# Optimization experiments

Measured on AMD Instinct MI355X. Metric: run time of the kernel, lower is better.

Reference implementation:

```python
import jax, jax.numpy as jnp
import numpy as np

MUL = 128
LS = [0, 1, 2]
D1 = [MUL * (2 * l + 1) for l in LS]            # per-irrep dims of x1 / out: 128, 384, 640
D2 = [2 * l + 1 for l in LS]                    # per-irrep dims of x2 (mul=1): 1, 3, 5
O1 = np.concatenate([[0], np.cumsum(D1)])       # offsets into x1 / out
O2 = np.concatenate([[0], np.cumsum(D2)])       # offsets into x2
PATHS = [(l1, l2, lo) for l1 in LS for l2 in LS for lo in LS
         if abs(l1 - l2) <= lo <= l1 + l2]      # 15 sorted 'uvw' instructions
DIM_OUT = int(sum(D1))

def _count():
    # fan-in count per output position: each 'uvw' path adds mul_1*mul_2 = 128
    c = np.zeros(DIM_OUT, dtype=np.float32)
    for (_, _, lo) in PATHS:
        c[O1[lo]:O1[lo] + D1[lo]] += MUL * 1
    return np.maximum(c, 1.0)

COUNT = jnp.asarray(_count())

def setup_inputs() -> dict:
    key = jax.random.key(0)
    ks = jax.random.split(key, 3 + len(PATHS))
    N = 16384
    inp = {
        "x1": jax.random.normal(ks[0], (N, int(sum(D1))), jnp.float32),
        "x2": jax.random.normal(ks[1], (N, int(sum(D2))), jnp.float32),
        "ws": jax.random.normal(ks[2], (len(PATHS), MUL, 1, MUL), jnp.float32),
    }
    for p, (l1, l2, lo) in enumerate(PATHS):
        inp[f"c{p}"] = jax.random.normal(ks[3 + p], (2 * l1 + 1, 2 * l2 + 1, 2 * lo + 1), jnp.float32)
    return inp

def _forward(x1, x2, ws, cs):
    N = x1.shape[0]
    out = jnp.zeros((N, DIM_OUT), x1.dtype)
    for p, (l1, l2, lo) in enumerate(PATHS):
        # s1: [N, mul1, 2l1+1]; s2: [N, mul2=1, 2l2+1]
        s1 = x1[:, int(O1[l1]):int(O1[l1] + D1[l1])].reshape(N, MUL, 2 * l1 + 1)
        s2 = x2[:, int(O2[l2]):int(O2[l2] + D2[l2])].reshape(N, 1, 2 * l2 + 1)
        # weighted CG contraction: ws[p] [u,v,w], cs[p] [i,j,k]
        contrib = jnp.einsum('uvw,ijk,zui,zvj->zwk', ws[p], cs[p], s1, s2)
        out = out.at[:, int(O1[lo]):int(O1[lo] + D1[lo])].add(contrib.reshape(N, D1[lo]))
    # fan-in (component) normalization
    return out / jnp.sqrt(COUNT)

def reference(x1, x2, ws, c0, c1, c2, c3, c4, c5, c6, c7, c8, c9, c10, c11, c12, c13, c14):
    cs = [c0, c1, c2, c3, c4, c5, c6, c7, c8, c9, c10, c11, c12, c13, c14]
    return _forward(x1, x2, ws, cs)
```

## Files before the change

### kernel.cpp

```cpp
#include <hip/hip_runtime.h>
#include <hip/hip_bf16.h>

typedef float f32x4 __attribute__((ext_vector_type(4)));
typedef short bf16x8 __attribute__((ext_vector_type(8)));

#define ZT 16
#define TL_COLS 160
#define TL_RING (TL_COLS * 128)
#define YL_BUF 640

constexpr int cL1[15]  = {0,0,0,1,1,1,1,1,1,2,2,2,2,2,2};
constexpr int cL2[15]  = {0,1,2,0,1,1,1,2,2,0,1,1,2,2,2};
constexpr int cLO[15]  = {0,1,2,1,0,1,2,1,2,2,1,2,0,1,2};
constexpr int cCSZ[15] = {1,9,25,9,9,27,45,45,75,25,45,75,25,75,125};
constexpr int cCOFF[15]= {0,1,10,35,44,53,80,125,170,245,270,315,390,415,490};
constexpr int cO1[3] = {0,128,512};
constexpr int cO2[3] = {0,1,4};

constexpr int cSEQ[15] = {0,4,12, 1,3,5,7,10,13, 2,6,8,9,11,14};

struct CP { const float* p[15]; };

__device__ __forceinline__ ushort f2bf(float f) {
    union { __hip_bfloat16 h; ushort u; } c;
    c.h = __float2bfloat16(f);
    return c.u;
}

__global__ void prep_w(const float* __restrict__ ws, ushort* __restrict__ wb) {
    __shared__ float lds[64 * 132];
    const int p = blockIdx.x;
    const int tid = threadIdx.x;
    const float* src = ws + (size_t)p * 16384;
    ushort* dst = wb + (size_t)p * 16384;
    for (int half = 0; half < 2; ++half) {
        for (int i = tid; i < 8192; i += 256) {
            int u = i >> 7, w = i & 127;
            lds[u * 132 + w] = src[(half * 64 + u) * 128 + w];
        }
        __syncthreads();
        for (int i = tid; i < 8192; i += 256) {
            int w = i >> 6, u = i & 63;
            dst[w * 128 + half * 64 + u] = f2bf(lds[u * 132 + w]);
        }
        __syncthreads();
    }
}

template<int P>
__device__ __forceinline__ void compute_y(int tid, const float* __restrict__ cl,
                                          const float* __restrict__ x2l,
                                          float* __restrict__ ybuf) {
    constexpr int l2 = cL2[P], lo = cLO[P];
    constexpr int d1 = 2*cL1[P]+1, d2 = 2*l2+1, dO = 2*lo+1;
    constexpr int ipad = (d1 == 5) ? 8 : 4;
    constexpr int span_pad = dO * ipad;
    constexpr int ny = ZT * span_pad;
    for (int idx = tid; idx < ny; idx += 256) {
        const int z = idx / span_pad, rem = idx - z * span_pad;
        const int k = rem / ipad, i = rem & (ipad - 1);
        float s = 0.f;
        if (i < d1) {
            #pragma unroll
            for (int j = 0; j < d2; ++j)
                s += cl[cCOFF[P] + (i*d2 + j)*dO + k] * x2l[z*9 + cO2[l2] + j];
        }
        ybuf[idx] = s;
    }
}

template<int L1>
__device__ __forceinline__ void load_x1(const float* __restrict__ x1, int z0,
                                        int wv, int lane, float (&x1c)[4][2][5]) {
    #pragma unroll
    for (int r = 0; r < 4; ++r) {
        const float* b = x1 + (size_t)(z0 + wv*4 + r) * 1152;
        if constexpr (L1 == 0) {
            const float2 t = *reinterpret_cast<const float2*>(b + 2*lane);
            x1c[r][0][0] = t.x; x1c[r][1][0] = t.y;
        } else if constexpr (L1 == 1) {
            float f6[6];
            #pragma unroll
            for (int j = 0; j < 3; ++j) {
                const float2 t = *reinterpret_cast<const float2*>(b + 128 + 6*lane + 2*j);
                f6[2*j] = t.x; f6[2*j + 1] = t.y;
            }
            #pragma unroll
            for (int i = 0; i < 3; ++i) { x1c[r][0][i] = f6[i]; x1c[r][1][i] = f6[3+i]; }
        } else {
            float f10[10];
            #pragma unroll
            for (int j = 0; j < 5; ++j) {
                const float2 t = *reinterpret_cast<const float2*>(b + 512 + 10*lane + 2*j);
                f10[2*j] = t.x; f10[2*j + 1] = t.y;
            }
            #pragma unroll
            for (int i = 0; i < 5; ++i) { x1c[r][0][i] = f10[i]; x1c[r][1][i] = f10[5+i]; }
        }
    }
}

template<int S>
__device__ __forceinline__ void path_iter(
    int tid, const float* __restrict__ x1, int z0,
    const ushort* __restrict__ Wb, const float* __restrict__ Wsrc, int use_prep,
    float (&x1c)[4][2][5],
    float* __restrict__ yl, ushort* __restrict__ Tl,
    const float* __restrict__ cl, const float* __restrict__ x2l,
    f32x4 (&acc)[5][2])
{
    constexpr int P = cSEQ[S];
    constexpr int l1 = cL1[P], lo = cLO[P];
    constexpr int d1 = 2*l1+1, dO = 2*lo+1;
    constexpr int ipad = (d1 == 5) ? 8 : 4;
    constexpr int span_pad = dO * ipad;
    constexpr int roff = (S & 1) ? 80 : 0;
    const int lane = tid & 63, wv = tid >> 6;
    const int g = lane >> 4, m = lane & 15;

    ushort* Tcur = Tl + roff * 128;
    const float* ycur = yl + (S & 1) * YL_BUF;

    if constexpr (S == 0 || cL1[cSEQ[S - 1]] != l1)
        load_x1<l1>(x1, z0, wv, lane, x1c);

    {
        const int u0 = 2 * lane;
        #pragma unroll
        for (int r = 0; r < 4; ++r) {
            const int z = wv * 4 + r;
            #pragma unroll
            for (int k = 0; k < dO; ++k) {
                const f32x4 y0 = *reinterpret_cast<const f32x4*>(
                    ycur + z * span_pad + k * ipad);
                float s0 = 0.f, s1 = 0.f;
                #pragma unroll
                for (int i = 0; i < ((d1 < 4) ? d1 : 4); ++i) {
                    s0 += x1c[r][0][i] * y0[i];
                    s1 += x1c[r][1][i] * y0[i];
                }
                if constexpr (d1 == 5) {
                    const float y4 = ycur[z * span_pad + k * ipad + 4];
                    s0 += x1c[r][0][4] * y4;
                    s1 += x1c[r][1][4] * y4;
                }
                const int col = z * dO + k;
                union { uint u32; ushort h[2]; } pk;
                pk.h[0] = f2bf(s0);
                pk.h[1] = f2bf(s1);
                const uint idx = (uint)(col * 128 + u0) ^ (uint)((col & 7) << 3);
                *reinterpret_cast<uint*>(Tcur + idx) = pk.u32;
            }
        }
    }

    bf16x8 aP[2][4];
    if (use_prep) {
        const ushort* wp = Wb + P * 16384;
        #pragma unroll
        for (int nt = 0; nt < 2; ++nt)
        #pragma unroll
        for (int ks = 0; ks < 4; ++ks)
            aP[nt][ks] = *reinterpret_cast<const bf16x8*>(
                wp + (wv*32 + nt*16 + m)*128 + ks*32 + g*8);
    } else {
        const float* wp = Wsrc + P * 16384;
        #pragma unroll
        for (int nt = 0; nt < 2; ++nt)
        #pragma unroll
        for (int ks = 0; ks < 4; ++ks) {
            bf16x8 v;
            #pragma unroll
            for (int e = 0; e < 8; ++e)
                v[e] = (short)f2bf(wp[(ks*32 + g*8 + e)*128 + wv*32 + nt*16 + m]);
            aP[nt][ks] = v;
        }
    }

    if constexpr (S < 14)
        compute_y<cSEQ[S + 1]>(tid, cl, x2l, yl + ((S + 1) & 1) * YL_BUF);

    __syncthreads();

    #pragma unroll
    for (int t = 0; t < dO; ++t) {
        #pragma unroll
        for (int ks = 0; ks < 4; ++ks) {
            const uint idx = (uint)((t*16 + m) * 128 + ks*32 + g*8)
                           ^ (uint)(((t*16 + m) & 7) << 3);
            const bf16x8 a = *reinterpret_cast<const bf16x8*>(Tcur + idx);
            acc[t][0] = __builtin_amdgcn_mfma_f32_16x16x32_bf16(a, aP[0][ks], acc[t][0], 0,0,0);
            acc[t][1] = __builtin_amdgcn_mfma_f32_16x16x32_bf16(a, aP[1][ks], acc[t][1], 0,0,0);
        }
    }
}

template<int LO, bool LAST>
__device__ __forceinline__ void store_pass(const f32x4 (&acc)[5][2], float* __restrict__ out,
                                           float* __restrict__ stage, int z0, int tid)
{
    constexpr int dO = 2*LO + 1;
    constexpr float scale = (LO == 0) ? 0.05103103630798288f
                                      : 0.03608439182435161f;
    const int lane = tid & 63, wv = tid >> 6;
    const int g = lane >> 4, m = lane & 15;
    __syncthreads();
    #pragma unroll
    for (int t = 0; t < dO; ++t)
    #pragma unroll
    for (int r = 0; r < 4; ++r) {
        const int zcol = t*16 + g*4 + r;
        const int z = zcol / dO, k = zcol - z*dO;
        #pragma unroll
        for (int nt = 0; nt < 2; ++nt) {
            const int w = wv*32 + nt*16 + m;
            stage[z*(128*dO) + w*dO + k] = acc[t][nt][r] * scale;
        }
    }
    __syncthreads();
    const float4* src = (const float4*)stage;
    #pragma unroll
    for (int it = 0; it < 2*dO; ++it) {
        const int idx = it * 256 + tid;
        const int z = idx / (32*dO), rem = idx - z*(32*dO);
        ((float4*)(out + (size_t)(z0 + z)*1152 + cO1[LO]))[rem] = src[idx];
    }
    if constexpr (!LAST) __syncthreads();
}

__device__ __forceinline__ void zero_acc(f32x4 (&acc)[5][2]) {
    #pragma unroll
    for (int t = 0; t < 5; ++t)
        #pragma unroll
        for (int nt = 0; nt < 2; ++nt)
            acc[t][nt] = (f32x4){0.f, 0.f, 0.f, 0.f};
}

__global__ __launch_bounds__(256, 2)
void tp_main(const float* __restrict__ x1, const float* __restrict__ x2,
             const float* __restrict__ wsrc, const ushort* __restrict__ wb,
             int use_prep, CP cp, float* __restrict__ out)
{
    __shared__ __align__(16) ushort Tl[TL_RING];
    __shared__ __align__(16) float yl[2 * YL_BUF];
    __shared__ float cl[615];
    __shared__ float x2l[ZT * 9];

    const int tid = threadIdx.x;
    const int z0 = blockIdx.x * ZT;

    #pragma unroll
    for (int p = 0; p < 15; ++p)
        for (int i = tid; i < cCSZ[p]; i += 256) cl[cCOFF[p] + i] = cp.p[p][i];
    for (int i = tid; i < ZT * 9; i += 256) x2l[i] = x2[(size_t)z0 * 9 + i];

    float x1c[4][2][5];
    f32x4 acc[5][2];
    zero_acc(acc);

    __syncthreads();
    compute_y<cSEQ[0]>(tid, cl, x2l, yl);
    __syncthreads();

    float* stage = (float*)Tl;

    path_iter< 0>(tid, x1, z0, wb, wsrc, use_prep, x1c, yl, Tl, cl, x2l, acc);
    path_iter< 1>(tid, x1, z0, wb, wsrc, use_prep, x1c, yl, Tl, cl, x2l, acc);
    path_iter< 2>(tid, x1, z0, wb, wsrc, use_prep, x1c, yl, Tl, cl, x2l, acc);
    store_pass<0, false>(acc, out, stage, z0, tid);
    zero_acc(acc);

    path_iter< 3>(tid, x1, z0, wb, wsrc, use_prep, x1c, yl, Tl, cl, x2l, acc);
    path_iter< 4>(tid, x1, z0, wb, wsrc, use_prep, x1c, yl, Tl, cl, x2l, acc);
    path_iter< 5>(tid, x1, z0, wb, wsrc, use_prep, x1c, yl, Tl, cl, x2l, acc);
    path_iter< 6>(tid, x1, z0, wb, wsrc, use_prep, x1c, yl, Tl, cl, x2l, acc);
    path_iter< 7>(tid, x1, z0, wb, wsrc, use_prep, x1c, yl, Tl, cl, x2l, acc);
    path_iter< 8>(tid, x1, z0, wb, wsrc, use_prep, x1c, yl, Tl, cl, x2l, acc);
    store_pass<1, false>(acc, out, stage, z0, tid);
    zero_acc(acc);

    path_iter< 9>(tid, x1, z0, wb, wsrc, use_prep, x1c, yl, Tl, cl, x2l, acc);
    path_iter<10>(tid, x1, z0, wb, wsrc, use_prep, x1c, yl, Tl, cl, x2l, acc);
    path_iter<11>(tid, x1, z0, wb, wsrc, use_prep, x1c, yl, Tl, cl, x2l, acc);
    path_iter<12>(tid, x1, z0, wb, wsrc, use_prep, x1c, yl, Tl, cl, x2l, acc);
    path_iter<13>(tid, x1, z0, wb, wsrc, use_prep, x1c, yl, Tl, cl, x2l, acc);
    path_iter<14>(tid, x1, z0, wb, wsrc, use_prep, x1c, yl, Tl, cl, x2l, acc);
    store_pass<2, true>(acc, out, stage, z0, tid);
}

extern "C" void kernel_launch(void* const* d_in, const int* in_sizes, int n_in,
                              void* d_out, int out_size, void* d_ws, size_t ws_size,
                              hipStream_t stream) {
    const float* x1 = (const float*)d_in[0];
    const float* x2 = (const float*)d_in[1];
    const float* ws = (const float*)d_in[2];
    CP cp;
    for (int p = 0; p < 15; ++p) cp.p[p] = (const float*)d_in[3 + p];
    float* out = (float*)d_out;

    const int N = in_sizes[0] / 1152;
    const int use_prep = (ws_size >= (size_t)(15 * 128 * 128 * 2)) ? 1 : 0;

    if (use_prep)
        prep_w<<<15, 256, 0, stream>>>(ws, (ushort*)d_ws);
    tp_main<<<N / ZT, 256, 0, stream>>>(x1, x2, ws, (const ushort*)d_ws,
                                        use_prep, cp, out);
}
```

Measured before the change: 104.9 us.

## Stream weight fragments per k-slice and raise occupancy to three blocks per SU

Replaces the eight preloaded weight fragments per stage with a two-register double buffer that fetches the next k-slice while the current one feeds the MFMAs, and reorders the loop to go over k-slices first. The x1 load for the next stage's l1 now happens before the barrier instead of at the start of the next stage. Launch bounds ask for three blocks per CU instead of two. The aim is to cut VGPR pressure so occupancy can rise and global latency can be hidden. In exchange, weight loads now sit on the MFMA critical path, and the tighter register cap may cause spills.

After: 121.4 us. 1.16x slower.

```diff
diff --git a/kernel.cpp b/kernel.cpp
--- a/kernel.cpp
+++ b/kernel.cpp
@@ -121,7 +121,7 @@
     ushort* Tcur = Tl + roff * 128;
     const float* ycur = yl + (S & 1) * YL_BUF;
 
-    if constexpr (S == 0 || cL1[cSEQ[S - 1]] != l1)
+    if constexpr (S == 0)
         load_x1<l1>(x1, z0, wv, lane, x1c);
 
     {
@@ -154,44 +154,61 @@
         }
     }
 
-    bf16x8 aP[2][4];
+    bf16x8 aQ0, aQ1;
     if (use_prep) {
         const ushort* wp = Wb + P * 16384;
-        #pragma unroll
-        for (int nt = 0; nt < 2; ++nt)
-        #pragma unroll
-        for (int ks = 0; ks < 4; ++ks)
-            aP[nt][ks] = *reinterpret_cast<const bf16x8*>(
-                wp + (wv*32 + nt*16 + m)*128 + ks*32 + g*8);
+        aQ0 = *reinterpret_cast<const bf16x8*>(wp + (wv*32 + m)*128 + g*8);
+        aQ1 = *reinterpret_cast<const bf16x8*>(wp + (wv*32 + 16 + m)*128 + g*8);
     } else {
         const float* wp = Wsrc + P * 16384;
-        #pragma unroll
-        for (int nt = 0; nt < 2; ++nt)
-        #pragma unroll
-        for (int ks = 0; ks < 4; ++ks) {
-            bf16x8 v;
-            #pragma unroll
-            for (int e = 0; e < 8; ++e)
-                v[e] = (short)f2bf(wp[(ks*32 + g*8 + e)*128 + wv*32 + nt*16 + m]);
-            aP[nt][ks] = v;
-        }
+        bf16x8 v0, v1;
+        #pragma unroll
+        for (int e = 0; e < 8; ++e) {
+            v0[e] = (short)f2bf(wp[(g*8 + e)*128 + wv*32 + m]);
+            v1[e] = (short)f2bf(wp[(g*8 + e)*128 + wv*32 + 16 + m]);
+        }
+        aQ0 = v0; aQ1 = v1;
     }
 
     if constexpr (S < 14)
         compute_y<cSEQ[S + 1]>(tid, cl, x2l, yl + ((S + 1) & 1) * YL_BUF);
 
-    __syncthreads();
-
-    #pragma unroll
-    for (int t = 0; t < dO; ++t) {
-        #pragma unroll
-        for (int ks = 0; ks < 4; ++ks) {
+    if constexpr (S < 14) {
+        constexpr int nl1 = cL1[cSEQ[S + 1]];
+        if constexpr (nl1 != l1)
+            load_x1<nl1>(x1, z0, wv, lane, x1c);
+    }
+
+    __syncthreads();
+
+    #pragma unroll
+    for (int ks = 0; ks < 4; ++ks) {
+        bf16x8 aN0, aN1;
+        if (ks < 3) {
+            if (use_prep) {
+                const ushort* wp = Wb + P * 16384;
+                aN0 = *reinterpret_cast<const bf16x8*>(wp + (wv*32 + m)*128 + (ks+1)*32 + g*8);
+                aN1 = *reinterpret_cast<const bf16x8*>(wp + (wv*32 + 16 + m)*128 + (ks+1)*32 + g*8);
+            } else {
+                const float* wp = Wsrc + P * 16384;
+                bf16x8 v0, v1;
+                #pragma unroll
+                for (int e = 0; e < 8; ++e) {
+                    v0[e] = (short)f2bf(wp[((ks+1)*32 + g*8 + e)*128 + wv*32 + m]);
+                    v1[e] = (short)f2bf(wp[((ks+1)*32 + g*8 + e)*128 + wv*32 + 16 + m]);
+                }
+                aN0 = v0; aN1 = v1;
+            }
+        }
+        #pragma unroll
+        for (int t = 0; t < dO; ++t) {
             const uint idx = (uint)((t*16 + m) * 128 + ks*32 + g*8)
                            ^ (uint)(((t*16 + m) & 7) << 3);
             const bf16x8 a = *reinterpret_cast<const bf16x8*>(Tcur + idx);
-            acc[t][0] = __builtin_amdgcn_mfma_f32_16x16x32_bf16(a, aP[0][ks], acc[t][0], 0,0,0);
-            acc[t][1] = __builtin_amdgcn_mfma_f32_16x16x32_bf16(a, aP[1][ks], acc[t][1], 0,0,0);
-        }
+            acc[t][0] = __builtin_amdgcn_mfma_f32_16x16x32_bf16(a, aQ0, acc[t][0], 0,0,0);
+            acc[t][1] = __builtin_amdgcn_mfma_f32_16x16x32_bf16(a, aQ1, acc[t][1], 0,0,0);
+        }
+        if (ks < 3) { aQ0 = aN0; aQ1 = aN1; }
     }
 }
 
@@ -236,7 +253,7 @@
             acc[t][nt] = (f32x4){0.f, 0.f, 0.f, 0.f};
 }
 
-__global__ __launch_bounds__(256, 2)
+__global__ __launch_bounds__(256, 3)
 void tp_main(const float* __restrict__ x1, const float* __restrict__ x2,
              const float* __restrict__ wsrc, const ushort* __restrict__ wb,
              int use_prep, CP cp, float* __restrict__ out)
```
